# Kernel optimization log

Hardware: AMD Instinct MI355X
Metric: run time of the kernel (lower is better)

## Reference

```python
import jax, jax.numpy as jnp
import numpy as np

E, V, F, D = 500000, 50000, 100000, 128

def setup_inputs() -> dict:
    key = jax.random.key(0)
    ks = jax.random.split(key, 8)
    return {
        "prev_m_f_to_v": jax.random.normal(ks[0], (E, D), jnp.float32),
        "variable": jax.random.normal(ks[1], (V, D), jnp.float32),
        "factor": jax.random.normal(ks[2], (F, D), jnp.float32),
        "edge_attr": jax.random.normal(ks[3], (E, D), jnp.float32),
        "v_to_f": jax.random.randint(ks[4], (E,), 0, V, jnp.int32),
        "f_to_v": jax.random.randint(ks[5], (E,), 0, F, jnp.int32),
        "Wv": jax.random.normal(ks[6], (3 * D, D), jnp.float32) * (1.0 / np.sqrt(3 * D)),
        "bv": jnp.zeros((D,), jnp.float32),
        "Wf": jax.random.normal(ks[7], (3 * D, D), jnp.float32) * (1.0 / np.sqrt(3 * D)),
        "bf": jnp.zeros((D,), jnp.float32),
    }

def _mlp(x, y, edge_attr, W, b):
    # update(): concat along features then Linear(3d->d) + relu
    h = jnp.concatenate((x, y, edge_attr), axis=-1)  # [E, 3D]
    return jax.nn.relu(h @ W + b)                    # [E, D]

def reference(prev_m_f_to_v, variable, factor, edge_attr, v_to_f, f_to_v, Wv, bv, Wf, bf):
    nV = variable.shape[0]
    nF = factor.shape[0]
    # scatter-sum of factor->variable messages onto variables
    sum_f_to_v = jax.ops.segment_sum(prev_m_f_to_v, v_to_f, num_segments=nV)  # [V, D]
    # BP exclusion: gather back and subtract own message
    m_v_to_f = sum_f_to_v[v_to_f] - prev_m_f_to_v                             # [E, D]
    m_v_to_f = _mlp(variable[v_to_f], m_v_to_f, edge_attr, Wv, bv)            # [E, D]
    # scatter-sum of variable->factor messages onto factors
    sum_v_to_f = jax.ops.segment_sum(m_v_to_f, f_to_v, num_segments=nF)       # [F, D]
    m_f_to_v = sum_v_to_f[f_to_v] - m_v_to_f                                  # [E, D]
    m_f_to_v = _mlp(factor[f_to_v], m_f_to_v, edge_attr, Wf, bf)              # [E, D]
    new_factor = sum_v_to_f + factor
    new_variable = sum_f_to_v + variable
    return (m_f_to_v, new_factor, new_variable)
```

## Files before the change

### kernel.cpp

```cpp
#include <hip/hip_runtime.h>

typedef __attribute__((ext_vector_type(8))) __bf16 bf16x8;
typedef __attribute__((ext_vector_type(4))) __bf16 bf16x4;
typedef __attribute__((ext_vector_type(2))) __bf16 bf16x2;
typedef __attribute__((ext_vector_type(4))) float f32x4;

__device__ inline bf16x8 pack8(f32x4 u0, f32x4 u1) {
    bf16x8 r;
    r[0] = (__bf16)u0[0]; r[1] = (__bf16)u0[1]; r[2] = (__bf16)u0[2]; r[3] = (__bf16)u0[3];
    r[4] = (__bf16)u1[0]; r[5] = (__bf16)u1[1]; r[6] = (__bf16)u1[2]; r[7] = (__bf16)u1[3];
    return r;
}

__global__ void pack_all(const float* __restrict__ Wv, const float* __restrict__ Wf,
                         __bf16* __restrict__ Wtab_v, __bf16* __restrict__ Wedge_v,
                         __bf16* __restrict__ Wtab_f, __bf16* __restrict__ Wedge_f) {
    int which = blockIdx.x >> 7;
    int i = ((blockIdx.x & 127) << 8) + threadIdx.x;
    const float* W = (which < 2) ? Wv : Wf;
    __bf16* out = (which == 0) ? Wtab_v : (which == 1) ? Wedge_v
                 : (which == 2) ? Wtab_f : Wedge_f;
    int baseA = (which & 1) ? 128 : 0;
    float sA  = (which & 1) ? -1.f : 1.f;
    int baseB = (which & 1) ? 256 : 128;
    int k = i >> 7, d = i & 127;
    float v = (k < 128) ? sA * W[(long)(baseA + k) * 128 + d]
                        : W[(long)(baseB + (k - 128)) * 128 + d];
    int t = k >> 5, n = d >> 4;
    int lane = (d & 15) | (((k >> 3) & 3) << 4);
    int j = k & 7;
    out[((long)(t * 8 + n) * 64 + lane) * 8 + j] = (__bf16)v;
}

__global__ __launch_bounds__(256) void conv_eattr(
    const float* __restrict__ e, __bf16* __restrict__ efrag, int E, int nunits) {
    int gw = (int)(((long)blockIdx.x * blockDim.x + threadIdx.x) >> 6);
    if (gw >= nunits) return;
    int lane = threadIdx.x & 63;
    long row = (long)(gw >> 2) * 16 + (lane & 15);
    if (row >= E) row = E - 1;
    int k0 = (gw & 3) * 32 + (lane >> 4) * 8;
    const float* p = e + row * 128 + k0;
    f32x4 u0 = *(const f32x4*)p;
    f32x4 u1 = *(const f32x4*)(p + 4);
    *(bf16x8*)(efrag + (long)gw * 512 + lane * 8) = pack8(u0, u1);
}


__global__ void hist_kernel(const int* __restrict__ v_to_f, const int* __restrict__ f_to_v,
                            int* __restrict__ counts, int V, int E) {
    int stride = gridDim.x * blockDim.x;
    for (int e = blockIdx.x * blockDim.x + threadIdx.x; e < E; e += stride) {
        atomicAdd(&counts[v_to_f[e]], 1);
        atomicAdd(&counts[V + f_to_v[e]], 1);
    }
}

#define SCAN_BLOCK 256
#define SCAN_ELEMS 4

__global__ void scan_pass1(const int* __restrict__ counts, int* __restrict__ partials, int N) {
    int t = threadIdx.x;
    int base = blockIdx.x * (SCAN_BLOCK * SCAN_ELEMS) + t * SCAN_ELEMS;
    int s = 0;
#pragma unroll
    for (int j = 0; j < SCAN_ELEMS; ++j) {
        int i = base + j;
        if (i < N) s += counts[i];
    }
#pragma unroll
    for (int off = 1; off < 64; off <<= 1) s += __shfl_xor(s, off);
    __shared__ int lds[4];
    if ((t & 63) == 0) lds[t >> 6] = s;
    __syncthreads();
    if (t == 0) partials[blockIdx.x] = lds[0] + lds[1] + lds[2] + lds[3];
}

__global__ void scan_pass3(const int* __restrict__ counts, const int* __restrict__ partials,
                           int* __restrict__ offsets, int* __restrict__ cursors,
                           int N, int total) {
    int t = threadIdx.x;
    int pre = 0;
    for (int i = 0; i < (int)blockIdx.x; ++i) pre += partials[i];
    int base = blockIdx.x * (SCAN_BLOCK * SCAN_ELEMS) + t * SCAN_ELEMS;
    int c[SCAN_ELEMS];
    int s = 0;
#pragma unroll
    for (int j = 0; j < SCAN_ELEMS; ++j) {
        int i = base + j;
        c[j] = (i < N) ? counts[i] : 0;
        s += c[j];
    }
    int lane = t & 63, w = t >> 6;
    int x = s;
#pragma unroll
    for (int off = 1; off < 64; off <<= 1) { int y = __shfl_up(x, off); if (lane >= off) x += y; }
    __shared__ int lds[4];
    if (lane == 63) lds[w] = x;
    __syncthreads();
    int add = 0;
    for (int i = 0; i < w; ++i) add += lds[i];
    int run = x + add - s + pre;
#pragma unroll
    for (int j = 0; j < SCAN_ELEMS; ++j) {
        int i = base + j;
        if (i < N) { offsets[i] = run; cursors[i] = run; }
        run += c[j];
    }
    if (blockIdx.x == 0 && t == 0) offsets[N] = total;
}

__global__ void fill_kernel(const int* __restrict__ v_to_f, const int* __restrict__ f_to_v,
                            int* __restrict__ cursors, int* __restrict__ bucket, int V, int E) {
    int stride = gridDim.x * blockDim.x;
    for (int e = blockIdx.x * blockDim.x + threadIdx.x; e < E; e += stride) {
        int p = atomicAdd(&cursors[v_to_f[e]], 1);
        bucket[p] = e;
        int q = atomicAdd(&cursors[V + f_to_v[e]], 1);
        bucket[q] = e;
    }
}


__global__ __launch_bounds__(256) void gsum_f32(
    const float* __restrict__ src, const int* __restrict__ bucket,
    const int* __restrict__ offsets, int toff,
    float* __restrict__ sumout, __bf16* __restrict__ prevbf, int T) {
    int gw = (int)((blockIdx.x * (long)blockDim.x + threadIdx.x) >> 6);
    if (gw >= T) return;
    int lane = threadIdx.x & 63;
    int start = offsets[toff + gw], end = offsets[toff + gw + 1];
    float ax = 0.f, ay = 0.f, bx = 0.f, by = 0.f;
    float cx = 0.f, cy = 0.f, dx = 0.f, dy = 0.f;
    int i = start;
    for (; i + 3 < end; i += 4) {
        int e0 = bucket[i], e1 = bucket[i + 1], e2 = bucket[i + 2], e3 = bucket[i + 3];
        float2 v0 = *(const float2*)(src + (long)e0 * 128 + lane * 2);
        float2 v1 = *(const float2*)(src + (long)e1 * 128 + lane * 2);
        float2 v2 = *(const float2*)(src + (long)e2 * 128 + lane * 2);
        float2 v3 = *(const float2*)(src + (long)e3 * 128 + lane * 2);
        bf16x2 b0, b1, b2, b3;
        b0[0] = (__bf16)v0.x; b0[1] = (__bf16)v0.y;
        b1[0] = (__bf16)v1.x; b1[1] = (__bf16)v1.y;
        b2[0] = (__bf16)v2.x; b2[1] = (__bf16)v2.y;
        b3[0] = (__bf16)v3.x; b3[1] = (__bf16)v3.y;
        *(bf16x2*)(prevbf + (long)e0 * 128 + lane * 2) = b0;
        *(bf16x2*)(prevbf + (long)e1 * 128 + lane * 2) = b1;
        *(bf16x2*)(prevbf + (long)e2 * 128 + lane * 2) = b2;
        *(bf16x2*)(prevbf + (long)e3 * 128 + lane * 2) = b3;
        ax += v0.x; ay += v0.y; bx += v1.x; by += v1.y;
        cx += v2.x; cy += v2.y; dx += v3.x; dy += v3.y;
    }
    for (; i < end; ++i) {
        int e0 = bucket[i];
        float2 v0 = *(const float2*)(src + (long)e0 * 128 + lane * 2);
        bf16x2 b0;
        b0[0] = (__bf16)v0.x; b0[1] = (__bf16)v0.y;
        *(bf16x2*)(prevbf + (long)e0 * 128 + lane * 2) = b0;
        ax += v0.x; ay += v0.y;
    }
    ax += bx + cx + dx; ay += by + cy + dy;
    long o = (long)gw * 128 + lane * 2;
    *(float2*)(sumout + o) = make_float2(ax, ay);
}

__global__ __launch_bounds__(256) void gsum_bf16(
    const __bf16* __restrict__ src, const int* __restrict__ bucket,
    const int* __restrict__ offsets, int toff,
    float* __restrict__ sumout, int T) {
    int gw = (int)((blockIdx.x * (long)blockDim.x + threadIdx.x) >> 6);
    if (gw >= T) return;
    int lane = threadIdx.x & 63;
    int start = offsets[toff + gw], end = offsets[toff + gw + 1];
    float ax = 0.f, ay = 0.f, bx = 0.f, by = 0.f;
    float cx = 0.f, cy = 0.f, dx = 0.f, dy = 0.f;
    int i = start;
    for (; i + 3 < end; i += 4) {
        int e0 = bucket[i], e1 = bucket[i + 1], e2 = bucket[i + 2], e3 = bucket[i + 3];
        bf16x2 v0 = *(const bf16x2*)(src + (long)e0 * 128 + lane * 2);
        bf16x2 v1 = *(const bf16x2*)(src + (long)e1 * 128 + lane * 2);
        bf16x2 v2 = *(const bf16x2*)(src + (long)e2 * 128 + lane * 2);
        bf16x2 v3 = *(const bf16x2*)(src + (long)e3 * 128 + lane * 2);
        ax += (float)v0[0]; ay += (float)v0[1]; bx += (float)v1[0]; by += (float)v1[1];
        cx += (float)v2[0]; cy += (float)v2[1]; dx += (float)v3[0]; dy += (float)v3[1];
    }
    for (; i < end; ++i) {
        int e0 = bucket[i];
        bf16x2 v0 = *(const bf16x2*)(src + (long)e0 * 128 + lane * 2);
        ax += (float)v0[0]; ay += (float)v0[1];
    }
    ax += bx + cx + dx; ay += by + cy + dy;
    long o = (long)gw * 128 + lane * 2;
    *(float2*)(sumout + o) = make_float2(ax, ay);
}

__global__ __launch_bounds__(256, 4) void table_gemm(
    const float* __restrict__ src0, const float* __restrict__ src1,
    const __bf16* __restrict__ WT, const float* __restrict__ bias,
    __bf16* __restrict__ out, float* __restrict__ addout, int T) {
    const int wave = threadIdx.x >> 6;
    const int lane = threadIdx.x & 63;
    const int row = lane & 15;
    const int kch = lane >> 4;
    const long wbase = ((long)blockIdx.x * 4 + wave) * 32;

    const float* p0[2]; const float* p1[2];
#pragma unroll
    for (int rb = 0; rb < 2; ++rb) {
        long r = wbase + rb * 16 + row;
        long rl = (r < T) ? r : (T - 1);
        p0[rb] = src0 + rl * 128 + kch * 8;
        p1[rb] = src1 + rl * 128 + kch * 8;
    }

    f32x4 acc[8][2];
#pragma unroll
    for (int n = 0; n < 8; ++n) {
        acc[n][0] = (f32x4){0.f, 0.f, 0.f, 0.f};
        acc[n][1] = (f32x4){0.f, 0.f, 0.f, 0.f};
    }

#pragma unroll
    for (int t = 0; t < 8; ++t) {
        bf16x8 a[2];
#pragma unroll
        for (int rb = 0; rb < 2; ++rb) {
            const float* p = (t < 4) ? (p0[rb] + t * 32) : (p1[rb] + (t - 4) * 32);
            f32x4 u0 = *(const f32x4*)p;
            f32x4 u1 = *(const f32x4*)(p + 4);
            a[rb] = pack8(u0, u1);
        }
        const __bf16* bbase = WT + (long)t * 8 * 512 + lane * 8;
#pragma unroll
        for (int n = 0; n < 8; ++n) {
            bf16x8 b = *(const bf16x8*)(bbase + n * 512);
            acc[n][0] = __builtin_amdgcn_mfma_f32_16x16x32_bf16(a[0], b, acc[n][0], 0, 0, 0);
            acc[n][1] = __builtin_amdgcn_mfma_f32_16x16x32_bf16(a[1], b, acc[n][1], 0, 0, 0);
        }
    }

    const int colbase = lane & 15;
    const int orow = (lane >> 4) * 4;
#pragma unroll
    for (int n = 0; n < 8; ++n) {
        int col = n * 16 + colbase;
        float bz = bias[col];
#pragma unroll
        for (int rb = 0; rb < 2; ++rb)
#pragma unroll
            for (int rr = 0; rr < 4; ++rr) {
                long r = wbase + rb * 16 + orow + rr;
                if (r < T) out[r * 128 + col] = (__bf16)(acc[n][rb][rr] + bz);
            }
    }

    const long eb = (long)blockIdx.x * 128 * 128;
#pragma unroll
    for (int j = 0; j < 16; ++j) {
        int vec = j * 256 + threadIdx.x;
        long r = (long)blockIdx.x * 128 + (vec >> 5);
        if (r < T) {
            long off = eb + (long)vec * 4;
            f32x4 x = *(const f32x4*)(src0 + off);
            f32x4 y = *(const f32x4*)(src1 + off);
            f32x4 o;
            o[0] = x[0] + y[0]; o[1] = x[1] + y[1];
            o[2] = x[2] + y[2]; o[3] = x[3] + y[3];
            *(f32x4*)(addout + off) = o;
        }
    }
}

template <int PHASE>
__global__ __launch_bounds__(256, 4) void edge_gemm(
    const __bf16* __restrict__ arow, const __bf16* __restrict__ efrag,
    const __bf16* __restrict__ WT, const __bf16* __restrict__ G,
    const int* __restrict__ idx, __bf16* __restrict__ outb,
    float* __restrict__ outf, int E) {
    __shared__ char lds[4][8192];
    const int wave = threadIdx.x >> 6;
    const int lane = threadIdx.x & 63;
    const int l16 = lane & 15;
    const int kch = lane >> 4;
    const long wrow = (long)blockIdx.x * 64 + wave * 16;
    const long maxtile = (long)(E - 1) >> 4;

    long rA = wrow + l16; if (rA >= E) rA = E - 1;
    long tile = wrow >> 4; if (tile > maxtile) tile = maxtile;

    auto loadA = [&](int t) -> bf16x8 {
        if (t < 4) return *(const bf16x8*)(arow + rA * 128 + t * 32 + kch * 8);
        return *(const bf16x8*)(efrag + (tile * 4 + (t - 4)) * 512 + lane * 8);
    };

    f32x4 acc[8];
#pragma unroll
    for (int n = 0; n < 8; ++n) acc[n] = (f32x4){0.f, 0.f, 0.f, 0.f};

    bf16x8 a_cur = loadA(0);
#pragma unroll
    for (int t = 0; t < 8; ++t) {
        bf16x8 a_nxt;
        if (t < 7) a_nxt = loadA(t + 1);
        const __bf16* bbase = WT + (long)t * 4096 + lane * 8;
#pragma unroll
        for (int n = 0; n < 8; ++n) {
            bf16x8 b = *(const bf16x8*)(bbase + n * 512);
            acc[n] = __builtin_amdgcn_mfma_f32_16x16x32_bf16(a_cur, b, acc[n], 0, 0, 0);
        }
        a_cur = a_nxt;
    }

    float* lbuf = (float*)&lds[wave][0];
    const int slotcol = lane & 31;
    const int rhalf = lane >> 5;
#pragma unroll
    for (int n = 0; n < 8; ++n)
#pragma unroll
        for (int rr = 0; rr < 4; ++rr) {
            int row = kch * 4 + rr;
            int col = n * 16 + l16;
            int slot = col >> 2;
            lbuf[row * 128 + (((slot ^ (row & 7)) << 2) | (col & 3))] = acc[n][rr];
        }
#pragma unroll
    for (int j = 0; j < 8; ++j) {
        int row = 2 * j + rhalf;
        long eo = wrow + row;
        f32x4 v = *(const f32x4*)&lbuf[row * 128 + ((slotcol ^ (row & 7)) << 2)];
        if (eo < E) {
            int g = idx[eo];
            bf16x4 gb = *(const bf16x4*)(G + (long)g * 128 + slotcol * 4);
            f32x4 o;
#pragma unroll
            for (int i = 0; i < 4; ++i) {
                float x = v[i] + (float)gb[i];
                o[i] = x > 0.f ? x : 0.f;
            }
            if (PHASE == 1) {
                bf16x4 ob;
#pragma unroll
                for (int i = 0; i < 4; ++i) ob[i] = (__bf16)o[i];
                *(bf16x4*)(outb + eo * 128 + slotcol * 4) = ob;
            } else {
                *(f32x4*)(outf + eo * 128 + slotcol * 4) = o;
            }
        }
    }
}

extern "C" void kernel_launch(void* const* d_in, const int* in_sizes, int n_in,
                              void* d_out, int out_size, void* d_ws, size_t ws_size,
                              hipStream_t stream) {
    const float* prev_m   = (const float*)d_in[0];
    const float* variable = (const float*)d_in[1];
    const float* factor   = (const float*)d_in[2];
    const float* eattr    = (const float*)d_in[3];
    const int*   v_to_f   = (const int*)d_in[4];
    const int*   f_to_v   = (const int*)d_in[5];
    const float* Wv       = (const float*)d_in[6];
    const float* bv       = (const float*)d_in[7];
    const float* Wf       = (const float*)d_in[8];
    const float* bf       = (const float*)d_in[9];

    const int E = in_sizes[0] / 128;
    const int V = in_sizes[1] / 128;
    const int F = in_sizes[2] / 128;
    const int NT = V + F;
    const int eblocks64 = (E + 63) / 64;
    const int ntiles = (E + 15) / 16;
    const int nunits = ntiles * 4;

    float* out_m        = (float*)d_out;
    float* out_factor   = out_m + (long)E * 128;
    float* out_variable = out_factor + (long)F * 128;

    char* ws = (char*)d_ws;
    float* sum_f_to_v = (float*)ws;  ws += (long)V * 128 * 4;
    float* sum_v_to_f = (float*)ws;  ws += (long)F * 128 * 4;
    __bf16* m1        = (__bf16*)ws; ws += (long)E * 128 * 2;
    __bf16* prev_bf   = (__bf16*)ws; ws += (long)E * 128 * 2;
    __bf16* efrag     = (__bf16*)ws; ws += (long)nunits * 512 * 2;
    __bf16* G1        = (__bf16*)ws; ws += (long)V * 128 * 2;
    __bf16* G2        = (__bf16*)ws; ws += (long)F * 128 * 2;
    __bf16* Wtab_v    = (__bf16*)ws; ws += 256 * 128 * 2;
    __bf16* Wedge_v   = (__bf16*)ws; ws += 256 * 128 * 2;
    __bf16* Wtab_f    = (__bf16*)ws; ws += 256 * 128 * 2;
    __bf16* Wedge_f   = (__bf16*)ws; ws += 256 * 128 * 2;
    int* counts       = (int*)ws;    ws += (long)NT * 4;
    int* offsets      = (int*)ws;    ws += (long)(NT + 1) * 4;
    int* cursors      = (int*)ws;    ws += (long)NT * 4;
    int* bucket       = (int*)ws;    ws += (long)2 * E * 4;
    int* partials     = (int*)ws;    ws += 256 * 4;

    hipMemsetAsync(counts, 0, (size_t)NT * 4, stream);

    pack_all<<<dim3(512), dim3(256), 0, stream>>>(Wv, Wf, Wtab_v, Wedge_v, Wtab_f, Wedge_f);

    conv_eattr<<<dim3((nunits + 3) / 4), dim3(256), 0, stream>>>(eattr, efrag, E, nunits);

    hist_kernel<<<dim3(2048), dim3(256), 0, stream>>>(v_to_f, f_to_v, counts, V, E);
    int nb = (NT + SCAN_BLOCK * SCAN_ELEMS - 1) / (SCAN_BLOCK * SCAN_ELEMS);
    scan_pass1<<<dim3(nb), dim3(SCAN_BLOCK), 0, stream>>>(counts, partials, NT);
    scan_pass3<<<dim3(nb), dim3(SCAN_BLOCK), 0, stream>>>(counts, partials, offsets, cursors,
                                                          NT, 2 * E);
    fill_kernel<<<dim3(2048), dim3(256), 0, stream>>>(v_to_f, f_to_v, cursors, bucket, V, E);

    gsum_f32<<<dim3((V + 3) / 4), dim3(256), 0, stream>>>(
        prev_m, bucket, offsets, 0, sum_f_to_v, prev_bf, V);

    table_gemm<<<dim3((V + 127) / 128), dim3(256), 0, stream>>>(
        variable, sum_f_to_v, Wtab_v, bv, G1, out_variable, V);

    edge_gemm<1><<<dim3(eblocks64), dim3(256), 0, stream>>>(
        prev_bf, efrag, Wedge_v, G1, v_to_f, m1, nullptr, E);

    gsum_bf16<<<dim3((F + 3) / 4), dim3(256), 0, stream>>>(
        m1, bucket, offsets, V, sum_v_to_f, F);

    table_gemm<<<dim3((F + 127) / 128), dim3(256), 0, stream>>>(
        factor, sum_v_to_f, Wtab_f, bf, G2, out_factor, F);

    edge_gemm<2><<<dim3(eblocks64), dim3(256), 0, stream>>>(
        m1, efrag, Wedge_f, G2, f_to_v, nullptr, out_m, E);
}
```

Baseline: 798.2 us.

## Fuse fp32-to-bf16 conversion of edge_attr and prev messages into edge GEMM

Removes the separate conv_eattr kernel and the bf16 copy of prev_m written inside gsum_f32. The edge GEMMs now read fp32 edge_attr (and fp32 prev_m in phase 1) straight from global memory and pack them to bf16 in registers. This saves the intermediate bf16 writes and a kernel launch, but edge_attr is now read in fp32 twice, once per phase, at double the bytes. The occupancy hint also goes from 4 to 6 blocks per CU to help hide the extra load latency.

Result: faster. 727.0 us (-8.9%).

```diff
diff --git a/kernel.cpp b/kernel.cpp
--- a/kernel.cpp
+++ b/kernel.cpp
@@ -32,20 +32,6 @@
     out[((long)(t * 8 + n) * 64 + lane) * 8 + j] = (__bf16)v;
 }
 
-__global__ __launch_bounds__(256) void conv_eattr(
-    const float* __restrict__ e, __bf16* __restrict__ efrag, int E, int nunits) {
-    int gw = (int)(((long)blockIdx.x * blockDim.x + threadIdx.x) >> 6);
-    if (gw >= nunits) return;
-    int lane = threadIdx.x & 63;
-    long row = (long)(gw >> 2) * 16 + (lane & 15);
-    if (row >= E) row = E - 1;
-    int k0 = (gw & 3) * 32 + (lane >> 4) * 8;
-    const float* p = e + row * 128 + k0;
-    f32x4 u0 = *(const f32x4*)p;
-    f32x4 u1 = *(const f32x4*)(p + 4);
-    *(bf16x8*)(efrag + (long)gw * 512 + lane * 8) = pack8(u0, u1);
-}
-
 
 __global__ void hist_kernel(const int* __restrict__ v_to_f, const int* __restrict__ f_to_v,
                             int* __restrict__ counts, int V, int E) {
@@ -125,7 +111,7 @@
 __global__ __launch_bounds__(256) void gsum_f32(
     const float* __restrict__ src, const int* __restrict__ bucket,
     const int* __restrict__ offsets, int toff,
-    float* __restrict__ sumout, __bf16* __restrict__ prevbf, int T) {
+    float* __restrict__ sumout, int T) {
     int gw = (int)((blockIdx.x * (long)blockDim.x + threadIdx.x) >> 6);
     if (gw >= T) return;
     int lane = threadIdx.x & 63;
@@ -139,24 +125,12 @@
         float2 v1 = *(const float2*)(src + (long)e1 * 128 + lane * 2);
         float2 v2 = *(const float2*)(src + (long)e2 * 128 + lane * 2);
         float2 v3 = *(const float2*)(src + (long)e3 * 128 + lane * 2);
-        bf16x2 b0, b1, b2, b3;
-        b0[0] = (__bf16)v0.x; b0[1] = (__bf16)v0.y;
-        b1[0] = (__bf16)v1.x; b1[1] = (__bf16)v1.y;
-        b2[0] = (__bf16)v2.x; b2[1] = (__bf16)v2.y;
-        b3[0] = (__bf16)v3.x; b3[1] = (__bf16)v3.y;
-        *(bf16x2*)(prevbf + (long)e0 * 128 + lane * 2) = b0;
-        *(bf16x2*)(prevbf + (long)e1 * 128 + lane * 2) = b1;
-        *(bf16x2*)(prevbf + (long)e2 * 128 + lane * 2) = b2;
-        *(bf16x2*)(prevbf + (long)e3 * 128 + lane * 2) = b3;
         ax += v0.x; ay += v0.y; bx += v1.x; by += v1.y;
         cx += v2.x; cy += v2.y; dx += v3.x; dy += v3.y;
     }
     for (; i < end; ++i) {
         int e0 = bucket[i];
         float2 v0 = *(const float2*)(src + (long)e0 * 128 + lane * 2);
-        bf16x2 b0;
-        b0[0] = (__bf16)v0.x; b0[1] = (__bf16)v0.y;
-        *(bf16x2*)(prevbf + (long)e0 * 128 + lane * 2) = b0;
         ax += v0.x; ay += v0.y;
     }
     ax += bx + cx + dx; ay += by + cy + dy;
@@ -272,25 +246,34 @@
 }
 
 template <int PHASE>
-__global__ __launch_bounds__(256, 4) void edge_gemm(
-    const __bf16* __restrict__ arow, const __bf16* __restrict__ efrag,
-    const __bf16* __restrict__ WT, const __bf16* __restrict__ G,
-    const int* __restrict__ idx, __bf16* __restrict__ outb,
-    float* __restrict__ outf, int E) {
+__global__ __launch_bounds__(256, 6) void edge_gemm(
+    const float* __restrict__ arowf, const __bf16* __restrict__ arowb,
+    const float* __restrict__ eattr, const __bf16* __restrict__ WT,
+    const __bf16* __restrict__ G, const int* __restrict__ idx,
+    __bf16* __restrict__ outb, float* __restrict__ outf, int E) {
     __shared__ char lds[4][8192];
     const int wave = threadIdx.x >> 6;
     const int lane = threadIdx.x & 63;
     const int l16 = lane & 15;
     const int kch = lane >> 4;
     const long wrow = (long)blockIdx.x * 64 + wave * 16;
-    const long maxtile = (long)(E - 1) >> 4;
-
     long rA = wrow + l16; if (rA >= E) rA = E - 1;
-    long tile = wrow >> 4; if (tile > maxtile) tile = maxtile;
 
     auto loadA = [&](int t) -> bf16x8 {
-        if (t < 4) return *(const bf16x8*)(arow + rA * 128 + t * 32 + kch * 8);
-        return *(const bf16x8*)(efrag + (tile * 4 + (t - 4)) * 512 + lane * 8);
+        if (t < 4) {
+            if (PHASE == 1) {
+                const float* p = arowf + rA * 128 + t * 32 + kch * 8;
+                f32x4 u0 = *(const f32x4*)p;
+                f32x4 u1 = *(const f32x4*)(p + 4);
+                return pack8(u0, u1);
+            } else {
+                return *(const bf16x8*)(arowb + rA * 128 + t * 32 + kch * 8);
+            }
+        }
+        const float* p = eattr + rA * 128 + (t - 4) * 32 + kch * 8;
+        f32x4 u0 = *(const f32x4*)p;
+        f32x4 u1 = *(const f32x4*)(p + 4);
+        return pack8(u0, u1);
     };
 
     f32x4 acc[8];
@@ -368,8 +351,6 @@
     const int F = in_sizes[2] / 128;
     const int NT = V + F;
     const int eblocks64 = (E + 63) / 64;
-    const int ntiles = (E + 15) / 16;
-    const int nunits = ntiles * 4;
 
     float* out_m        = (float*)d_out;
     float* out_factor   = out_m + (long)E * 128;
@@ -379,8 +360,6 @@
     float* sum_f_to_v = (float*)ws;  ws += (long)V * 128 * 4;
     float* sum_v_to_f = (float*)ws;  ws += (long)F * 128 * 4;
     __bf16* m1        = (__bf16*)ws; ws += (long)E * 128 * 2;
-    __bf16* prev_bf   = (__bf16*)ws; ws += (long)E * 128 * 2;
-    __bf16* efrag     = (__bf16*)ws; ws += (long)nunits * 512 * 2;
     __bf16* G1        = (__bf16*)ws; ws += (long)V * 128 * 2;
     __bf16* G2        = (__bf16*)ws; ws += (long)F * 128 * 2;
     __bf16* Wtab_v    = (__bf16*)ws; ws += 256 * 128 * 2;
@@ -397,8 +376,6 @@
 
     pack_all<<<dim3(512), dim3(256), 0, stream>>>(Wv, Wf, Wtab_v, Wedge_v, Wtab_f, Wedge_f);
 
-    conv_eattr<<<dim3((nunits + 3) / 4), dim3(256), 0, stream>>>(eattr, efrag, E, nunits);
-
     hist_kernel<<<dim3(2048), dim3(256), 0, stream>>>(v_to_f, f_to_v, counts, V, E);
     int nb = (NT + SCAN_BLOCK * SCAN_ELEMS - 1) / (SCAN_BLOCK * SCAN_ELEMS);
     scan_pass1<<<dim3(nb), dim3(SCAN_BLOCK), 0, stream>>>(counts, partials, NT);
@@ -407,13 +384,13 @@
     fill_kernel<<<dim3(2048), dim3(256), 0, stream>>>(v_to_f, f_to_v, cursors, bucket, V, E);
 
     gsum_f32<<<dim3((V + 3) / 4), dim3(256), 0, stream>>>(
-        prev_m, bucket, offsets, 0, sum_f_to_v, prev_bf, V);
+        prev_m, bucket, offsets, 0, sum_f_to_v, V);
 
     table_gemm<<<dim3((V + 127) / 128), dim3(256), 0, stream>>>(
         variable, sum_f_to_v, Wtab_v, bv, G1, out_variable, V);
 
     edge_gemm<1><<<dim3(eblocks64), dim3(256), 0, stream>>>(
-        prev_bf, efrag, Wedge_v, G1, v_to_f, m1, nullptr, E);
+        prev_m, nullptr, eattr, Wedge_v, G1, v_to_f, m1, nullptr, E);
 
     gsum_bf16<<<dim3((F + 3) / 4), dim3(256), 0, stream>>>(
         m1, bucket, offsets, V, sum_v_to_f, F);
@@ -422,5 +399,5 @@
         factor, sum_v_to_f, Wtab_f, bf, G2, out_factor, F);
 
     edge_gemm<2><<<dim3(eblocks64), dim3(256), 0, stream>>>(
-        m1, efrag, Wedge_f, G2, f_to_v, nullptr, out_m, E);
-}
+        nullptr, m1, eattr, Wedge_f, G2, f_to_v, nullptr, out_m, E);
+}
```
